# Kernel tuning notes

Measured on AMD Instinct MI355X. Metric: run time of the kernel, lower is better.

The kernel has to match this reference:

```python
import jax, jax.numpy as jnp
import numpy as np

B, T, U, V = 8, 128, 64, 1024
BLANK = V - 1  # blank=-1 resolves to last class index


def setup_inputs() -> dict:
    key = jax.random.key(0)
    k1, k2, k3, k4 = jax.random.split(key, 4)
    logits = jax.random.normal(k1, (B, T, U + 1, V), dtype=jnp.float32)
    targets = jax.random.randint(k2, (B, U), 0, V - 1, dtype=jnp.int32)  # exclude blank
    logit_lengths = jax.random.randint(k3, (B,), T // 2, T + 1, dtype=jnp.int32)
    target_lengths = jax.random.randint(k4, (B,), U // 2, U + 1, dtype=jnp.int32)
    return {
        "logits": logits,
        "targets": targets,
        "logit_lengths": logit_lengths,
        "target_lengths": target_lengths,
    }


def _rnnt_neglogp(logits, targets, logit_lengths, target_lengths, blank):
    """RNNT forward-variable DP (Graves 2012). Returns per-sample -log p(y|x)."""
    Bn, Tn, U1, Vn = logits.shape
    Un = U1 - 1
    lp = jax.nn.log_softmax(logits, axis=-1)  # fused_log_softmax=True
    lp_blank = lp[..., blank]                                  # (B, T, U+1)
    idx = jnp.broadcast_to(targets[:, None, :, None], (Bn, Tn, Un, 1))
    lp_emit = jnp.take_along_axis(lp[:, :, :Un, :], idx, axis=-1)[..., 0]  # (B, T, U)

    # alpha[t, u]: log-prob of emitting first u labels using first t frames.
    # alpha[0, u] = sum_{v<u} emit(0, v)
    row0 = jnp.concatenate(
        [jnp.zeros((Bn, 1), lp.dtype), jnp.cumsum(lp_emit[:, 0, :], axis=-1)], axis=1
    )  # (B, U+1)

    def inner(a_prev, x):
        # a[u] = logaddexp(alpha[t-1,u] + blank(t-1,u),  a[u-1] + emit(t,u-1))
        b_u, e_u = x
        a_new = jnp.logaddexp(b_u, a_prev + e_u)
        return a_new, a_new

    def outer(prev_row, x):
        blank_prev, emit_t = x  # (B, U+1), (B, U)
        b_term = prev_row + blank_prev  # vertical (blank) transition term
        _, rest = jax.lax.scan(
            inner, b_term[:, 0], (b_term[:, 1:].T, emit_t.T)
        )  # rest: (U, B)
        new_row = jnp.concatenate([b_term[:, :1], rest.T], axis=1)  # (B, U+1)
        return new_row, new_row

    xs = (
        jnp.swapaxes(lp_blank[:, :-1, :], 0, 1),  # (T-1, B, U+1)
        jnp.swapaxes(lp_emit[:, 1:, :], 0, 1),    # (T-1, B, U)
    )
    _, rows = jax.lax.scan(outer, row0, xs)
    alpha = jnp.concatenate([row0[None], rows], axis=0)  # (T, B, U+1)

    bidx = jnp.arange(Bn)
    t_last = logit_lengths - 1
    u_last = target_lengths
    a_end = alpha[t_last, bidx, u_last]
    final_blank = lp_blank[bidx, t_last, u_last]
    return -(a_end + final_blank)


def reference(logits, targets, logit_lengths, target_lengths):
    return _rnnt_neglogp(logits, targets, logit_lengths, target_lengths, BLANK)
```

## Files before the change

kernel.cpp:

```cpp
#include <hip/hip_runtime.h>
#include <hip/hip_bf16.h>

#define BB 8
#define TT 128
#define UU 64
#define VV 1024
#define U1 65
#define NROWS (BB * TT * U1)
#define NDIAG (TT + UU)
#define DSZ (NDIAG * U1)
#define NPROD (NROWS / 4)
#define KPF 8

typedef unsigned long long ull;
#define SENT32 0xFFFFFFFFu

__device__ __forceinline__ float wave_sum64(float v) {
#pragma unroll
    for (int off = 32; off; off >>= 1) v += __shfl_xor(v, off, 64);
    return v;
}

__device__ __forceinline__ ull ldPu(const ull* Pb, int idx) {
    return __hip_atomic_load(Pb + idx, __ATOMIC_RELAXED, __HIP_MEMORY_SCOPE_AGENT);
}
__device__ __forceinline__ bool nrdy(ull v) {
    return ((unsigned)(v >> 32) == SENT32) | ((unsigned)v == SENT32);
}
__device__ __forceinline__ float2 u2f(ull v) {
    union { ull u; float2 f; } c; c.u = v; return c.f;
}

__global__ __launch_bounds__(256) void rnnt_fused_kernel(
    const float* __restrict__ logits, const int* __restrict__ targets,
    const int* __restrict__ logit_lengths, const int* __restrict__ target_lengths,
    ull* __restrict__ P, float* __restrict__ out) {

    if (blockIdx.x >= BB) {
        const int wave = threadIdx.x >> 6;
        const int lane = threadIdx.x & 63;
        const int row  = (blockIdx.x - BB) * 4 + wave;
        const int b   = row / (TT * U1);
        const int rem = row - b * (TT * U1);
        const int t   = rem / U1;
        const int u   = rem - t * U1;

        const float4* p4 = (const float4*)(logits + (size_t)row * VV);
        float4 x0 = p4[lane];
        float4 x1 = p4[lane + 64];
        float4 x2 = p4[lane + 128];
        float4 x3 = p4[lane + 192];

        float s = __expf(x0.x) + __expf(x0.y) + __expf(x0.z) + __expf(x0.w)
                + __expf(x1.x) + __expf(x1.y) + __expf(x1.z) + __expf(x1.w)
                + __expf(x2.x) + __expf(x2.y) + __expf(x2.z) + __expf(x2.w)
                + __expf(x3.x) + __expf(x3.y) + __expf(x3.z) + __expf(x3.w);
        s = wave_sum64(s);
        const float lse = __logf(s);

        const float blankv = __shfl(x3.w, 63, 64) - lse;
        float emitv = 0.f;
        if (u < UU) {
            const int tgt = targets[b * UU + u];
            const int qq = tgt >> 2, grp = qq >> 6, sl = qq & 63, c4 = tgt & 3;
            float4 g4 = (grp == 0) ? x0 : (grp == 1) ? x1 : (grp == 2) ? x2 : x3;
            float cv = (c4 == 0) ? g4.x : (c4 == 1) ? g4.y : (c4 == 2) ? g4.z : g4.w;
            emitv = __shfl(cv, sl, 64) - lse;
        }
        if (lane == 0) {
            union { ull u; float2 f; } pk;
            pk.f = make_float2(blankv, emitv);
            __hip_atomic_store(P + (size_t)b * DSZ + (t + u) * U1 + u, pk.u,
                               __ATOMIC_RELAXED, __HIP_MEMORY_SCOPE_AGENT);
        }
        return;
    }

    if (threadIdx.x >= 64) return;
    const int b = blockIdx.x;
    const int l = threadIdx.x;
    const ull* Pb = P + (size_t)b * DSZ;
    const int tl = logit_lengths[b] - 1;
    const int ul = target_lengths[b];
    const int Dfin = tl + ul;

    const float NEG = -1e30f;
    float aprev   = (l == 0) ? 0.f : NEG;
    float aprev64 = NEG;
    float res = 0.f;

    ull ring[KPF], ring64[KPF];
#pragma unroll
    for (int k = 0; k < KPF; ++k) {
        ring[k]   = ldPu(Pb, k * U1 + l);
        ring64[k] = ldPu(Pb, k * U1 + 64);
    }

    for (int base = 1; base <= NDIAG - 1; base += KPF) {
#pragma unroll
        for (int s = 0; s < KPF; ++s) {
            const int d = base + s;
            if (d > NDIAG - 1) break;
            const int c = d - 1;
            ull pu = ring[s], qu = ring64[s];
            const bool pex = (c >= l) && (c - l <= TT - 1);
            const bool qex = (c >= 64);
            int guard = 0;
            while (__ballot((pex && nrdy(pu)) || (qex && nrdy(qu)))) {
                pu = ldPu(Pb, c * U1 + l);
                qu = ldPu(Pb, c * U1 + 64);
                if (++guard > (1 << 18)) break;
            }
            float2 pr   = u2f(pu);
            float2 p64v = u2f(qu);
            float edl = __shfl_up(pr.y, 1, 64);
            float al  = __shfl_up(aprev, 1, 64);
            const int t = d - l;
            float va = (t >= 1) ? aprev + pr.x : NEG;
            float vb = (l >= 1) ? al + edl : NEG;
            float mm = fmaxf(va, vb);
            float r  = mm + __logf(__expf(va - mm) + __expf(vb - mm));
            r = (t >= 0 && t < TT) ? r : NEG;
            const int t64 = d - 64;
            float va64 = (t64 >= 1) ? aprev64 + p64v.x : NEG;
            float vb64 = aprev + pr.y;
            float mm64 = fmaxf(va64, vb64);
            float r64  = mm64 + __logf(__expf(va64 - mm64) + __expf(vb64 - mm64));
            r64 = (t64 >= 0) ? r64 : NEG;
            if (d == Dfin) {
                if (ul < 64) { if (l == ul) res = r; }
                else if (l == 63) res = r64;
            }
            aprev = r; aprev64 = r64;
            const int c2 = c + KPF;
            if (c2 <= NDIAG - 2) {
                ring[s]   = ldPu(Pb, c2 * U1 + l);
                ring64[s] = ldPu(Pb, c2 * U1 + 64);
            }
        }
    }

    const float rr = __shfl(res, (ul < 64) ? ul : 63, 64);
    if (l == 0) {
        ull v = ldPu(Pb, Dfin * U1 + ul);
        int guard = 0;
        while (nrdy(v) && ++guard < (1 << 18)) v = ldPu(Pb, Dfin * U1 + ul);
        out[b] = -(rr + u2f(v).x);
    }
}

extern "C" void kernel_launch(void* const* d_in, const int* in_sizes, int n_in,
                              void* d_out, int out_size, void* d_ws, size_t ws_size,
                              hipStream_t stream) {
    const float* logits         = (const float*)d_in[0];
    const int*   targets        = (const int*)d_in[1];
    const int*   logit_lengths  = (const int*)d_in[2];
    const int*   target_lengths = (const int*)d_in[3];
    float* outp = (float*)d_out;

    ull* P = (ull*)d_ws;

    hipMemsetAsync(P, 0xFF, (size_t)BB * DSZ * sizeof(ull), stream);
    rnnt_fused_kernel<<<BB + NPROD, 256, 0, stream>>>(
        logits, targets, logit_lengths, target_lengths, P, outp);
}
```

Measured before the change: 459.2 us.

## Make producer waves persistent with grid-stride loop and next-row prefetch

Replaces the one-wave-per-row producer launch with a fixed grid of 2040 blocks whose waves stride over rows, loading the next row's logits while computing the current row's log-softmax. This cuts block launch overhead and hides load latency behind the exp/reduction work. It changes the order in which rows are produced: later batches are finished only near the end, which can delay the DP consumer waves for those batches. It also uses more registers for the prefetched row.

```diff
diff --git a/kernel.cpp b/kernel.cpp
--- a/kernel.cpp
+++ b/kernel.cpp
@@ -9,7 +9,8 @@
 #define NROWS (BB * TT * U1)
 #define NDIAG (TT + UU)
 #define DSZ (NDIAG * U1)
-#define NPROD (NROWS / 4)
+#define NPBLK 2040
+#define NWAVES (NPBLK * 4)
 #define KPF 8
 
 typedef unsigned long long ull;
@@ -37,41 +38,55 @@
     ull* __restrict__ P, float* __restrict__ out) {
 
     if (blockIdx.x >= BB) {
-        const int wave = threadIdx.x >> 6;
         const int lane = threadIdx.x & 63;
-        const int row  = (blockIdx.x - BB) * 4 + wave;
-        const int b   = row / (TT * U1);
-        const int rem = row - b * (TT * U1);
-        const int t   = rem / U1;
-        const int u   = rem - t * U1;
+        const int wid  = (blockIdx.x - BB) * 4 + (threadIdx.x >> 6);
 
+        int row = wid;
         const float4* p4 = (const float4*)(logits + (size_t)row * VV);
-        float4 x0 = p4[lane];
-        float4 x1 = p4[lane + 64];
-        float4 x2 = p4[lane + 128];
-        float4 x3 = p4[lane + 192];
+        float4 x0 = p4[lane], x1 = p4[lane + 64],
+               x2 = p4[lane + 128], x3 = p4[lane + 192];
 
-        float s = __expf(x0.x) + __expf(x0.y) + __expf(x0.z) + __expf(x0.w)
-                + __expf(x1.x) + __expf(x1.y) + __expf(x1.z) + __expf(x1.w)
-                + __expf(x2.x) + __expf(x2.y) + __expf(x2.z) + __expf(x2.w)
-                + __expf(x3.x) + __expf(x3.y) + __expf(x3.z) + __expf(x3.w);
-        s = wave_sum64(s);
-        const float lse = __logf(s);
+        while (true) {
+            const int nrow = row + NWAVES;
+            const bool more = (nrow < NROWS);
+            float4 y0, y1, y2, y3;
+            if (more) {
+                const float4* q4 = (const float4*)(logits + (size_t)nrow * VV);
+                y0 = q4[lane]; y1 = q4[lane + 64];
+                y2 = q4[lane + 128]; y3 = q4[lane + 192];
+            }
 
-        const float blankv = __shfl(x3.w, 63, 64) - lse;
-        float emitv = 0.f;
-        if (u < UU) {
-            const int tgt = targets[b * UU + u];
-            const int qq = tgt >> 2, grp = qq >> 6, sl = qq & 63, c4 = tgt & 3;
-            float4 g4 = (grp == 0) ? x0 : (grp == 1) ? x1 : (grp == 2) ? x2 : x3;
-            float cv = (c4 == 0) ? g4.x : (c4 == 1) ? g4.y : (c4 == 2) ? g4.z : g4.w;
-            emitv = __shfl(cv, sl, 64) - lse;
-        }
-        if (lane == 0) {
-            union { ull u; float2 f; } pk;
-            pk.f = make_float2(blankv, emitv);
-            __hip_atomic_store(P + (size_t)b * DSZ + (t + u) * U1 + u, pk.u,
-                               __ATOMIC_RELAXED, __HIP_MEMORY_SCOPE_AGENT);
+            float s = __expf(x0.x) + __expf(x0.y) + __expf(x0.z) + __expf(x0.w)
+                    + __expf(x1.x) + __expf(x1.y) + __expf(x1.z) + __expf(x1.w)
+                    + __expf(x2.x) + __expf(x2.y) + __expf(x2.z) + __expf(x2.w)
+                    + __expf(x3.x) + __expf(x3.y) + __expf(x3.z) + __expf(x3.w);
+            s = wave_sum64(s);
+            const float lse = __logf(s);
+
+            const int b   = row / (TT * U1);
+            const int rem = row - b * (TT * U1);
+            const int t   = rem / U1;
+            const int u   = rem - t * U1;
+
+            const float blankv = __shfl(x3.w, 63, 64) - lse;
+            float emitv = 0.f;
+            if (u < UU) {
+                const int tgt = targets[b * UU + u];
+                const int qq = tgt >> 2, grp = qq >> 6, sl = qq & 63, c4 = tgt & 3;
+                float4 g4 = (grp == 0) ? x0 : (grp == 1) ? x1
+                          : (grp == 2) ? x2 : x3;
+                float cv = (c4 == 0) ? g4.x : (c4 == 1) ? g4.y
+                         : (c4 == 2) ? g4.z : g4.w;
+                emitv = __shfl(cv, sl, 64) - lse;
+            }
+            if (lane == 0) {
+                union { ull u; float2 f; } pk;
+                pk.f = make_float2(blankv, emitv);
+                __hip_atomic_store(P + (size_t)b * DSZ + (t + u) * U1 + u, pk.u,
+                                   __ATOMIC_RELAXED, __HIP_MEMORY_SCOPE_AGENT);
+            }
+            if (!more) break;
+            x0 = y0; x1 = y1; x2 = y2; x3 = y3; row = nrow;
         }
         return;
     }
@@ -161,6 +176,6 @@
     ull* P = (ull*)d_ws;
 
     hipMemsetAsync(P, 0xFF, (size_t)BB * DSZ * sizeof(ull), stream);
-    rnnt_fused_kernel<<<BB + NPROD, 256, 0, stream>>>(
+    rnnt_fused_kernel<<<BB + NPBLK, 256, 0, stream>>>(
         logits, targets, logit_lengths, target_lengths, P, outp);
 }
```

Result: no change. 461.4 us (+0.5%).
